# Optimization experiments

Hardware: AMD Instinct MI355X
Metric: run time of the kernel (lower is better)

Reference implementation:

```python
import jax, jax.numpy as jnp
import numpy as np

B, N, D = 2, 8192, 64          # batch, points, feature dim (dim_in == dim_out)
FILTER_SIZE = 11               # k nearest neighbors in feature space
N_ITER = 5                     # mean-field iterations


def setup_inputs() -> dict:
    key = jax.random.key(0)
    k0, k1, k2, k3 = jax.random.split(key, 4)
    return {
        "logits": jax.random.normal(k0, (B, N), jnp.float32),
        "p": jax.random.normal(k1, (B, D, N), jnp.float32),
        "W1": jax.random.normal(k2, (D, D), jnp.float32) / np.float32(np.sqrt(D)),
        "b1": jnp.zeros((D,), jnp.float32),
        "W2": jax.random.normal(k3, (D, D), jnp.float32) / np.float32(np.sqrt(D)),
        "b2": jnp.zeros((D,), jnp.float32),
    }


def reference(logits, p, W1, b1, W2, b2):
    # crf_encoder: two stacked Linear layers applied to p.permute(0,2,1) -> [B,N,D]
    f = jnp.einsum('bdn,de->bne', p, W1) + b1
    f = jnp.einsum('bne,ef->bnf', f, W2) + b2  # [B,N,D] feature embedding

    # pairwise squared distances in feature space: [B,N,N]
    sq = jnp.sum(f * f, axis=-1)
    d2 = sq[:, :, None] + sq[:, None, :] - 2.0 * jnp.einsum('bnd,bmd->bnm', f, f)

    # filter_size nearest neighbors (includes self) with Gaussian weights exp(-d2)
    neg_d2, idx = jax.lax.top_k(-d2, FILTER_SIZE)   # [B,N,K]
    w = jnp.exp(neg_d2)                             # [B,N,K]

    gather = jax.vmap(lambda qb, ib: qb[ib])        # per-batch gather: [N],[N,K]->[N,K]

    # mean-field iterations (binary CRF: sigmoid marginals, unary = logits)
    u = logits
    for _ in range(N_ITER):
        q = jax.nn.sigmoid(u)                       # current marginals [B,N]
        msg = jnp.sum(w * gather(q, idx), axis=-1)  # filtered message   [B,N]
        u = logits - msg                            # compatibility transform + unary

    return jax.nn.sigmoid(u)  # return_log_proba=False -> probabilities, [B,N]
```

## Files before the change

kernel.cpp:

```cpp
#include <hip/hip_runtime.h>

#define NPTS 8192
#define NTOT 16384
#define KNB 11
#define CAP 16
#define MARG 9.0f
#define MAXM 8192

typedef __attribute__((ext_vector_type(8))) short short8;
typedef __attribute__((ext_vector_type(4))) float f32x4;

__device__ __forceinline__ unsigned short f2bf(float x) {
  union { float f; unsigned u; } v; v.f = x;
  unsigned r = v.u + 0x7FFFu + ((v.u >> 16) & 1u);
  return (unsigned short)(r >> 16);
}

__device__ __forceinline__ float sigm(float x) { return 1.f / (1.f + expf(-x)); }

__global__ __launch_bounds__(256) void k0_w12(
    const float* __restrict__ W1, const float* __restrict__ b1,
    const float* __restrict__ W2, const float* __restrict__ b2,
    float* __restrict__ W12, float* __restrict__ b12,
    unsigned* __restrict__ cnt) {
  int t = blockIdx.x * 256 + threadIdx.x;
  cnt[t] = 0u;
  if (t >= 4096) return;
  int d = t >> 6, e = t & 63;
  float s = 0.f;
  for (int kk = 0; kk < 64; ++kk) s = fmaf(W1[d * 64 + kk], W2[kk * 64 + e], s);
  W12[t] = s;
  if (d == 0) {
    float sb = b2[e];
    for (int kk = 0; kk < 64; ++kk) sb = fmaf(b1[kk], W2[kk * 64 + e], sb);
    b12[e] = sb;
  }
}

__global__ __launch_bounds__(256) void k1_encode(
    const float* __restrict__ p,
    const float* __restrict__ W12,
    const float* __restrict__ b12,
    float* __restrict__ f32f,
    unsigned short* __restrict__ fpre,
    float* __restrict__ sq,
    float* __restrict__ sq32) {
  __shared__ float sp[64 * 64];
  __shared__ float sPart[4][64];
  int t = threadIdx.x, lane = t & 63;
  int w = __builtin_amdgcn_readfirstlane(t >> 6);
  int e0 = w * 16;
  int base = blockIdx.x * 64;
  int b = base >> 13, n0 = base & (NPTS - 1);
  const float* pb = p + (size_t)b * 64 * NPTS + n0;

  int row = t >> 4, chunk = t & 15;
#pragma unroll
  for (int k = 0; k < 4; ++k) {
    int r = k * 16 + row;
    uint4 v = *(const uint4*)(pb + (size_t)r * NPTS + chunk * 4);
    *(uint4*)(sp + r * 64 + chunk * 4) = v;
  }
  __syncthreads();

  float f[16];
#pragma unroll
  for (int j = 0; j < 16; ++j) f[j] = b12[e0 + j];

#pragma unroll 8
  for (int d = 0; d < 64; ++d) {
    float pd = sp[d * 64 + lane];
#pragma unroll
    for (int j = 0; j < 16; ++j)
      f[j] = fmaf(pd, W12[d * 64 + e0 + j], f[j]);
  }

  float s = 0.f;
#pragma unroll
  for (int j = 0; j < 16; ++j) s = fmaf(f[j], f[j], s);
  sPart[w][lane] = s;
  __syncthreads();
  if (w == 0) {
    float s32 = sPart[0][lane] + sPart[1][lane];
    float s64 = s32 + (sPart[2][lane] + sPart[3][lane]);
    sq32[base + lane] = s32;
    sq[base + lane] = s64;
  }

  f32x4* o4 = (f32x4*)(f32f + (size_t)(base + lane) * 64 + e0);
#pragma unroll
  for (int jj = 0; jj < 4; ++jj) {
    f32x4 v; v[0] = f[4 * jj]; v[1] = f[4 * jj + 1]; v[2] = f[4 * jj + 2]; v[3] = f[4 * jj + 3];
    o4[jj] = v;
  }
  if (w < 2) {
    unsigned* ob = (unsigned*)(fpre + (size_t)(base + lane) * 32 + e0);
#pragma unroll
    for (int jj = 0; jj < 8; ++jj) {
      unsigned lo = f2bf(f[2 * jj]);
      unsigned hi = f2bf(f[2 * jj + 1]);
      ob[jj] = lo | (hi << 16);
    }
  }
}

__global__ __launch_bounds__(256) void k2_gram_select(
    const unsigned short* __restrict__ fpre,
    const float* __restrict__ sq32,
    unsigned* __restrict__ cnt,
    unsigned* __restrict__ cand) {
  __shared__ uint4 sB[1024];
  int bid = blockIdx.x;
  int b = (bid >= 528) ? 1 : 0;
  int rem = bid - b * 528;
  int band = (int)((sqrtf(8.f * (float)rem + 1.f) - 1.f) * 0.5f);
  if (((band + 1) * (band + 2)) / 2 <= rem) band++;
  else if ((band * (band + 1)) / 2 > rem) band--;
  int seg = rem - (band * (band + 1)) / 2;

  int t = threadIdx.x;
  int lane = t & 63;
  int arow = lane & 15;
  int q = lane >> 4;
  int wave = t >> 6;
  int rowbase = band * 256 + wave * 64;
  int cbase = seg * 256;
  const unsigned short* fb = fpre + (size_t)b * NPTS * 32;
  const float* s32b = sq32 + b * NPTS;

  const uint4* gsrc = (const uint4*)fb + (size_t)seg * 1024;
  uint4 v[4];
#pragma unroll
  for (int k = 0; k < 4; ++k) v[k] = gsrc[t + k * 256];

  short8 afrag[4];
#pragma unroll
  for (int tr = 0; tr < 4; ++tr)
    afrag[tr] = *(const short8*)(fb + (size_t)(rowbase + tr * 16 + arow) * 32 + q * 8);

  f32x4 srq[4], hh[4];
#pragma unroll
  for (int tr = 0; tr < 4; ++tr) {
    srq[tr] = *(const f32x4*)(s32b + rowbase + tr * 16 + (q << 2));
    hh[tr] = 0.5f * srq[tr];
  }
  float thrc[16];
#pragma unroll
  for (int cc = 0; cc < 4; ++cc)
#pragma unroll
    for (int tc = 0; tc < 4; ++tc)
      thrc[cc * 4 + tc] = 0.5f * s32b[cbase + cc * 64 + tc * 16 + arow] - 0.5f * MARG;

#pragma unroll
  for (int k = 0; k < 4; ++k) {
    int c = t + k * 256;
    int r = c >> 2, qq = c & 3;
    sB[r * 4 + (qq ^ (r & 3))] = v[k];
  }
  __syncthreads();

  f32x4 z4 = {0.f, 0.f, 0.f, 0.f};
  unsigned hitmask = 0u;
#pragma unroll
  for (int cc = 0; cc < 4; ++cc)
#pragma unroll
    for (int tc = 0; tc < 4; ++tc) {
      int e = cc * 4 + tc;
      int rl = cc * 64 + tc * 16 + arow;
      short8 bf = *(const short8*)&sB[rl * 4 + (q ^ (rl & 3))];
      f32x4 a0 = __builtin_amdgcn_mfma_f32_16x16x32_bf16(afrag[0], bf, z4, 0, 0, 0);
      f32x4 a1 = __builtin_amdgcn_mfma_f32_16x16x32_bf16(afrag[1], bf, z4, 0, 0, 0);
      f32x4 a2 = __builtin_amdgcn_mfma_f32_16x16x32_bf16(afrag[2], bf, z4, 0, 0, 0);
      f32x4 a3 = __builtin_amdgcn_mfma_f32_16x16x32_bf16(afrag[3], bf, z4, 0, 0, 0);
      float m0 = fmaxf(fmaxf(a0[0] - hh[0][0], a0[1] - hh[0][1]),
                       fmaxf(a0[2] - hh[0][2], a0[3] - hh[0][3]));
      float m1 = fmaxf(fmaxf(a1[0] - hh[1][0], a1[1] - hh[1][1]),
                       fmaxf(a1[2] - hh[1][2], a1[3] - hh[1][3]));
      float m2 = fmaxf(fmaxf(a2[0] - hh[2][0], a2[1] - hh[2][1]),
                       fmaxf(a2[2] - hh[2][2], a2[3] - hh[2][3]));
      float m3 = fmaxf(fmaxf(a3[0] - hh[3][0], a3[1] - hh[3][1]),
                       fmaxf(a3[2] - hh[3][2], a3[3] - hh[3][3]));
      float m = fmaxf(fmaxf(m0, m1), fmaxf(m2, m3));
      if (__ballot(m > thrc[e])) hitmask |= (1u << e);
    }

  if (hitmask) {
#pragma unroll 1
    for (int e = 0; e < 16; ++e) {
      if (!(hitmask & (1u << e))) continue;
      int cc = e >> 2, tc = e & 3;
      int rl = cc * 64 + tc * 16 + arow;
      short8 bf = *(const short8*)&sB[rl * 4 + (q ^ (rl & 3))];
      int colpt = cbase + cc * 64 + tc * 16 + arow;
      float scv = s32b[colpt];
      f32x4 acc[4];
#pragma unroll
      for (int tr = 0; tr < 4; ++tr)
        acc[tr] = __builtin_amdgcn_mfma_f32_16x16x32_bf16(afrag[tr], bf, z4, 0, 0, 0);
#pragma unroll
      for (int tr = 0; tr < 4; ++tr)
#pragma unroll
        for (int rg = 0; rg < 4; ++rg) {
          float d2 = srq[tr][rg] + scv - 2.f * acc[tr][rg];
          if (d2 < MARG) {
            int rowpt = rowbase + tr * 16 + (q << 2) + rg;
            int gr = b * NPTS + rowpt;
            union { float f; unsigned u; } cv; cv.f = d2 + 16.f;
            unsigned kb = cv.u & 0xFFFFE000u;
            unsigned slot = atomicAdd(&cnt[gr], 1u);
            if (slot < CAP) cand[gr * CAP + slot] = kb | (unsigned)colpt;
            if (band != seg) {
              int gc = b * NPTS + colpt;
              unsigned slot2 = atomicAdd(&cnt[gc], 1u);
              if (slot2 < CAP) cand[gc * CAP + slot2] = kb | (unsigned)rowpt;
            }
          }
        }
    }
  }
}

__global__ __launch_bounds__(256) void k3_fused(
    const float* __restrict__ f32f, const float* __restrict__ sq,
    const unsigned* __restrict__ cnt, const unsigned* __restrict__ cand,
    float* __restrict__ Wbuf, int* __restrict__ IDXb,
    const float* __restrict__ logits, float* __restrict__ out) {
  int r = blockIdx.x * 256 + threadIdx.x;
  int b = r >> 13;
  unsigned count = cnt[r];
  if (count <= 1u) {
    float lg = logits[r];
    float u = lg;
#pragma unroll
    for (int it = 0; it < 5; ++it) u = lg - sigm(u);
    out[r] = sigm(u);
    return;
  }
  if (count > CAP) count = CAP;

  unsigned k[CAP];
#pragma unroll
  for (int j = 0; j < CAP; ++j)
    k[j] = (j < (int)count) ? cand[r * CAP + j] : 0xFFFFFFFFu;
#pragma unroll
  for (int a = 0; a < CAP - 1; ++a)
#pragma unroll
    for (int c = 0; c < CAP - 1; ++c) {
      unsigned lo = min(k[c], k[c + 1]);
      unsigned hi = max(k[c], k[c + 1]);
      k[c] = lo; k[c + 1] = hi;
    }

  float fr[64];
  const f32x4* fr4 = (const f32x4*)(f32f + (size_t)r * 64);
#pragma unroll
  for (int j = 0; j < 16; ++j) {
    f32x4 v = fr4[j];
    fr[4 * j] = v[0]; fr[4 * j + 1] = v[1]; fr[4 * j + 2] = v[2]; fr[4 * j + 3] = v[3];
  }
  float sqr = sq[r];
  int nsel = (int)count < KNB ? (int)count : KNB;
#pragma unroll
  for (int kk = 0; kk < KNB; ++kk) {
    float w = 0.f;
    int gi = r;
    if (kk < nsel) {
      int col = (int)(k[kk] & 8191u);
      gi = b * NPTS + col;
      const float* fm = f32f + (size_t)gi * 64;
      float dot = 0.f;
#pragma unroll
      for (int d = 0; d < 64; ++d) dot = fmaf(fr[d], fm[d], dot);
      float d2 = sqr + sq[gi] - 2.f * dot;
      w = expf(-d2);
    }
    Wbuf[(size_t)r * KNB + kk] = w;
    IDXb[(size_t)r * KNB + kk] = gi;
  }
}

__global__ __launch_bounds__(1024) void kt_iter(
    const unsigned* __restrict__ cnt,
    const float* __restrict__ Wbuf, const int* __restrict__ IDXb,
    const float* __restrict__ logits, float* __restrict__ out) {
  __shared__ float qs[NTOT];
  __shared__ int slist[MAXM];
  __shared__ float su[MAXM];
  __shared__ int sctr;
  int t = threadIdx.x;
  if (t == 0) sctr = 0;
  __syncthreads();

#pragma unroll 1
  for (int j = 0; j < 16; ++j) {
    int i = j * 1024 + t;
    if (cnt[i] > 1u) {
      qs[i] = sigm(logits[i]);
      int slot = atomicAdd(&sctr, 1);
      if (slot < MAXM) slist[slot] = i;
    }
  }
  __syncthreads();
  int nm = sctr; if (nm > MAXM) nm = MAXM;

  for (int it = 0; it < 5; ++it) {
#pragma unroll 1
    for (int k = t; k < nm; k += 1024) {
      int r = slist[k];
      float msg = 0.f;
      const float* wp = Wbuf + (size_t)r * KNB;
      const int* ip = IDXb + (size_t)r * KNB;
#pragma unroll
      for (int kk = 0; kk < KNB; ++kk) msg = fmaf(wp[kk], qs[ip[kk]], msg);
      su[k] = logits[r] - msg;
    }
    __syncthreads();
#pragma unroll 1
    for (int k = t; k < nm; k += 1024) qs[slist[k]] = sigm(su[k]);
    __syncthreads();
  }
#pragma unroll 1
  for (int k = t; k < nm; k += 1024) out[slist[k]] = sigm(su[k]);
}

extern "C" void kernel_launch(void* const* d_in, const int* in_sizes, int n_in,
                              void* d_out, int out_size, void* d_ws, size_t ws_size,
                              hipStream_t stream) {
  const float* logits = (const float*)d_in[0];
  const float* p      = (const float*)d_in[1];
  const float* W1     = (const float*)d_in[2];
  const float* b1     = (const float*)d_in[3];
  const float* W2     = (const float*)d_in[4];
  const float* b2     = (const float*)d_in[5];
  float* out = (float*)d_out;

  char* ws = (char*)d_ws;
  float* W12 = (float*)ws;
  float* b12 = W12 + 4096;
  float* f32f = b12 + 64;
  unsigned short* fpre = (unsigned short*)(f32f + (size_t)NTOT * 64);
  float* sq = (float*)(fpre + (size_t)NTOT * 32);
  float* sq32 = sq + NTOT;
  unsigned* cnt = (unsigned*)(sq32 + NTOT);
  unsigned* cand = cnt + NTOT;
  float* Wbuf = (float*)(cand + (size_t)NTOT * CAP);
  int* IDX = (int*)(Wbuf + (size_t)NTOT * KNB);

  k0_w12<<<64, 256, 0, stream>>>(W1, b1, W2, b2, W12, b12, cnt);
  k1_encode<<<256, 256, 0, stream>>>(p, W12, b12, f32f, fpre, sq, sq32);
  k2_gram_select<<<1056, 256, 0, stream>>>(fpre, sq32, cnt, cand);
  k3_fused<<<64, 256, 0, stream>>>(f32f, sq, cnt, cand, Wbuf, IDX, logits, out);
  kt_iter<<<1, 1024, 0, stream>>>(cnt, Wbuf, IDX, logits, out);
}
```

Baseline: 116.8 us.

## Fuse weight precompose into encoder and build active-row list during selection

Removes the separate W1*W2 precompose kernel. The encoder now applies the two linear layers in sequence through a padded shared-memory transpose and also zeroes the counters. The gram/select kernel appends each row to a global list the first time its count reaches two, so the single-block iteration kernel no longer scans all 16384 counters to build its work list. This trades one kernel launch and a serial scan for twice the encoder FLOPs and extra global atomics during selection.

```diff
diff --git a/kernel.cpp b/kernel.cpp
--- a/kernel.cpp
+++ b/kernel.cpp
@@ -18,34 +18,20 @@
 
 __device__ __forceinline__ float sigm(float x) { return 1.f / (1.f + expf(-x)); }
 
-__global__ __launch_bounds__(256) void k0_w12(
-    const float* __restrict__ W1, const float* __restrict__ b1,
-    const float* __restrict__ W2, const float* __restrict__ b2,
-    float* __restrict__ W12, float* __restrict__ b12,
-    unsigned* __restrict__ cnt) {
-  int t = blockIdx.x * 256 + threadIdx.x;
-  cnt[t] = 0u;
-  if (t >= 4096) return;
-  int d = t >> 6, e = t & 63;
-  float s = 0.f;
-  for (int kk = 0; kk < 64; ++kk) s = fmaf(W1[d * 64 + kk], W2[kk * 64 + e], s);
-  W12[t] = s;
-  if (d == 0) {
-    float sb = b2[e];
-    for (int kk = 0; kk < 64; ++kk) sb = fmaf(b1[kk], W2[kk * 64 + e], sb);
-    b12[e] = sb;
-  }
-}
-
 __global__ __launch_bounds__(256) void k1_encode(
     const float* __restrict__ p,
-    const float* __restrict__ W12,
-    const float* __restrict__ b12,
+    const float* __restrict__ W1,
+    const float* __restrict__ b1,
+    const float* __restrict__ W2,
+    const float* __restrict__ b2,
     float* __restrict__ f32f,
     unsigned short* __restrict__ fpre,
     float* __restrict__ sq,
-    float* __restrict__ sq32) {
+    float* __restrict__ sq32,
+    unsigned* __restrict__ cnt,
+    int* __restrict__ lctr) {
   __shared__ float sp[64 * 64];
+  __shared__ float st[64 * 65];
   __shared__ float sPart[4][64];
   int t = threadIdx.x, lane = t & 63;
   int w = __builtin_amdgcn_readfirstlane(t >> 6);
@@ -54,6 +40,9 @@
   int b = base >> 13, n0 = base & (NPTS - 1);
   const float* pb = p + (size_t)b * 64 * NPTS + n0;
 
+  if (w == 0) cnt[base + lane] = 0u;
+  if (base == 0 && t == 0) *lctr = 0;
+
   int row = t >> 4, chunk = t & 15;
 #pragma unroll
   for (int k = 0; k < 4; ++k) {
@@ -63,16 +52,29 @@
   }
   __syncthreads();
 
-  float f[16];
-#pragma unroll
-  for (int j = 0; j < 16; ++j) f[j] = b12[e0 + j];
-
+  float tt[16];
+#pragma unroll
+  for (int j = 0; j < 16; ++j) tt[j] = b1[e0 + j];
 #pragma unroll 8
   for (int d = 0; d < 64; ++d) {
     float pd = sp[d * 64 + lane];
 #pragma unroll
     for (int j = 0; j < 16; ++j)
-      f[j] = fmaf(pd, W12[d * 64 + e0 + j], f[j]);
+      tt[j] = fmaf(pd, W1[d * 64 + e0 + j], tt[j]);
+  }
+#pragma unroll
+  for (int j = 0; j < 16; ++j) st[lane * 65 + e0 + j] = tt[j];
+  __syncthreads();
+
+  float f[16];
+#pragma unroll
+  for (int j = 0; j < 16; ++j) f[j] = b2[e0 + j];
+#pragma unroll 8
+  for (int d = 0; d < 64; ++d) {
+    float td = st[lane * 65 + d];
+#pragma unroll
+    for (int j = 0; j < 16; ++j)
+      f[j] = fmaf(td, W2[d * 64 + e0 + j], f[j]);
   }
 
   float s = 0.f;
@@ -108,7 +110,9 @@
     const unsigned short* __restrict__ fpre,
     const float* __restrict__ sq32,
     unsigned* __restrict__ cnt,
-    unsigned* __restrict__ cand) {
+    unsigned* __restrict__ cand,
+    int* __restrict__ lctr,
+    int* __restrict__ list) {
   __shared__ uint4 sB[1024];
   int bid = blockIdx.x;
   int b = (bid >= 528) ? 1 : 0;
@@ -209,10 +213,18 @@
             unsigned kb = cv.u & 0xFFFFE000u;
             unsigned slot = atomicAdd(&cnt[gr], 1u);
             if (slot < CAP) cand[gr * CAP + slot] = kb | (unsigned)colpt;
+            if (slot == 1u) {
+              int ls = atomicAdd(lctr, 1);
+              if (ls < MAXM) list[ls] = gr;
+            }
             if (band != seg) {
               int gc = b * NPTS + colpt;
               unsigned slot2 = atomicAdd(&cnt[gc], 1u);
               if (slot2 < CAP) cand[gc * CAP + slot2] = kb | (unsigned)rowpt;
+              if (slot2 == 1u) {
+                int ls2 = atomicAdd(lctr, 1);
+                if (ls2 < MAXM) list[ls2] = gc;
+              }
             }
           }
         }
@@ -280,28 +292,22 @@
 }
 
 __global__ __launch_bounds__(1024) void kt_iter(
-    const unsigned* __restrict__ cnt,
+    const int* __restrict__ lctr, const int* __restrict__ list,
     const float* __restrict__ Wbuf, const int* __restrict__ IDXb,
     const float* __restrict__ logits, float* __restrict__ out) {
   __shared__ float qs[NTOT];
   __shared__ int slist[MAXM];
   __shared__ float su[MAXM];
-  __shared__ int sctr;
   int t = threadIdx.x;
-  if (t == 0) sctr = 0;
-  __syncthreads();
-
-#pragma unroll 1
-  for (int j = 0; j < 16; ++j) {
-    int i = j * 1024 + t;
-    if (cnt[i] > 1u) {
-      qs[i] = sigm(logits[i]);
-      int slot = atomicAdd(&sctr, 1);
-      if (slot < MAXM) slist[slot] = i;
-    }
-  }
-  __syncthreads();
-  int nm = sctr; if (nm > MAXM) nm = MAXM;
+  int nm = *lctr; if (nm > MAXM) nm = MAXM;
+
+#pragma unroll 1
+  for (int k = t; k < nm; k += 1024) {
+    int r = list[k];
+    slist[k] = r;
+    qs[r] = sigm(logits[r]);
+  }
+  __syncthreads();
 
   for (int it = 0; it < 5; ++it) {
 #pragma unroll 1
@@ -335,9 +341,7 @@
   float* out = (float*)d_out;
 
   char* ws = (char*)d_ws;
-  float* W12 = (float*)ws;
-  float* b12 = W12 + 4096;
-  float* f32f = b12 + 64;
+  float* f32f = (float*)ws;
   unsigned short* fpre = (unsigned short*)(f32f + (size_t)NTOT * 64);
   float* sq = (float*)(fpre + (size_t)NTOT * 32);
   float* sq32 = sq + NTOT;
@@ -345,10 +349,11 @@
   unsigned* cand = cnt + NTOT;
   float* Wbuf = (float*)(cand + (size_t)NTOT * CAP);
   int* IDX = (int*)(Wbuf + (size_t)NTOT * KNB);
-
-  k0_w12<<<64, 256, 0, stream>>>(W1, b1, W2, b2, W12, b12, cnt);
-  k1_encode<<<256, 256, 0, stream>>>(p, W12, b12, f32f, fpre, sq, sq32);
-  k2_gram_select<<<1056, 256, 0, stream>>>(fpre, sq32, cnt, cand);
+  int* lctr = IDX + (size_t)NTOT * KNB;
+  int* list = lctr + 1;
+
+  k1_encode<<<256, 256, 0, stream>>>(p, W1, b1, W2, b2, f32f, fpre, sq, sq32, cnt, lctr);
+  k2_gram_select<<<1056, 256, 0, stream>>>(fpre, sq32, cnt, cand, lctr, list);
   k3_fused<<<64, 256, 0, stream>>>(f32f, sq, cnt, cand, Wbuf, IDX, logits, out);
-  kt_iter<<<1, 1024, 0, stream>>>(cnt, Wbuf, IDX, logits, out);
-}
+  kt_iter<<<1, 1024, 0, stream>>>(lctr, list, Wbuf, IDX, logits, out);
+}
```

Result: faster. 111.8 us (-4.2%).
